# Optimization experiments

Hardware: AMD Instinct MI355X
Metric: run time of the kernel (lower is better)

## Reference

```python
import jax, jax.numpy as jnp
import numpy as np
import math

D = 768
H = 8
DK = D // H
FF = 1024
EPS = 1e-5


def _layer_norm(x, g, b):
    m = jnp.mean(x, axis=-1, keepdims=True)
    v = jnp.mean((x - m) ** 2, axis=-1, keepdims=True)
    return (x - m) * jax.lax.rsqrt(v + EPS) * g + b


def _mha(x, attention_mask, Wq, bq, Wv, bv, g, b):
    # x: (B,S,D); attention_mask: (B,S,1) bool (True = masked/padding query row)
    B, S, _ = x.shape
    q = (x @ Wq + bq).reshape(B, S, H, DK).transpose(0, 2, 1, 3)  # (B,H,S,dk)
    # NOTE: original code uses the V projection for BOTH k and v (k = self.V(x))
    kv = (x @ Wv + bv).reshape(B, S, H, DK).transpose(0, 2, 1, 3)
    k = kv
    v = kv
    w = jnp.einsum('bhqd,bhkd->bhqk', q, k) / math.sqrt(DK)  # (B,H,S,S)
    pad = attention_mask[:, None, :, :]                      # (B,1,S,1) -> bcast (B,1,S,S)
    causal = jnp.triu(jnp.ones((S, S), dtype=bool), k=1)     # look-ahead mask
    mask = pad | causal
    w = jnp.where(mask, jnp.float32(-1e9), w)
    # NOTE: original uses nn.Softmax(dim=2) -> softmax over the QUERY axis
    score = jax.nn.softmax(w, axis=2)
    o = jnp.einsum('bhqk,bhkd->bhqd', score, v)              # (B,H,S,dk)
    o = o.transpose(0, 2, 1, 3).reshape(B, S, D)
    return _layer_norm(o + x, g, b)


def _ffn(x, W1, b1, W2, b2, g, b):
    h = jax.nn.relu(x @ W1 + b1)
    return _layer_norm(h @ W2 + b2 + x, g, b)


def setup_inputs() -> dict:
    key = jax.random.key(0)
    ks = jax.random.split(key, 16)
    B, S = 8, 1024
    sc = 0.02
    inp = {
        'x': jax.random.normal(ks[0], (B, S, D), dtype=jnp.float32),
        'attention_mask': jax.random.randint(ks[1], (B, S, 1), 0, 2).astype(bool),
    }
    for i, pre in enumerate(['a1', 'a2']):
        inp[pre + '_Wq'] = jax.random.normal(ks[2 + 4 * i], (D, D), dtype=jnp.float32) * sc
        inp[pre + '_bq'] = jnp.zeros((D,), dtype=jnp.float32)
        inp[pre + '_Wv'] = jax.random.normal(ks[3 + 4 * i], (D, D), dtype=jnp.float32) * sc
        inp[pre + '_bv'] = jnp.zeros((D,), dtype=jnp.float32)
        inp[pre + '_g'] = jnp.ones((D,), dtype=jnp.float32)
        inp[pre + '_b'] = jnp.zeros((D,), dtype=jnp.float32)
    inp['f_W1'] = jax.random.normal(ks[10], (D, FF), dtype=jnp.float32) * sc
    inp['f_b1'] = jnp.zeros((FF,), dtype=jnp.float32)
    inp['f_W2'] = jax.random.normal(ks[11], (FF, D), dtype=jnp.float32) * sc
    inp['f_b2'] = jnp.zeros((D,), dtype=jnp.float32)
    inp['f_g'] = jnp.ones((D,), dtype=jnp.float32)
    inp['f_b'] = jnp.zeros((D,), dtype=jnp.float32)
    return inp


def reference(x, attention_mask,
              a1_Wq, a1_bq, a1_Wv, a1_bv, a1_g, a1_b,
              a2_Wq, a2_bq, a2_Wv, a2_bv, a2_g, a2_b,
              f_W1, f_b1, f_W2, f_b2, f_g, f_b):
    x = _mha(x, attention_mask, a1_Wq, a1_bq, a1_Wv, a1_bv, a1_g, a1_b)
    x = _mha(x, attention_mask, a2_Wq, a2_bq, a2_Wv, a2_bv, a2_g, a2_b)
    x = _ffn(x, f_W1, f_b1, f_W2, f_b2, f_g, f_b)
    return x
```

## Files before the change

### kernel.cpp

```cpp
#include <hip/hip_runtime.h>
#include <cstddef>

#define BB 8
#define SS 1024
#define DD 768
#define HH 8
#define DKK 96
#define FFF 1024
#define MM (BB*SS)
#define QVW 1536
#define SM_SCALE 0.10206207261596577f
#define NT2 8

typedef unsigned short ushort_t;
typedef short short8 __attribute__((ext_vector_type(8)));
typedef float f32x4 __attribute__((ext_vector_type(4)));
typedef float f32x16 __attribute__((ext_vector_type(16)));
typedef ushort_t us4 __attribute__((ext_vector_type(4)));
typedef unsigned uint2v __attribute__((ext_vector_type(2)));

__device__ __forceinline__ ushort_t f2b(float f) {
    union { float f; unsigned u; } x; x.f = f;
    unsigned r = x.u + 0x7fffu + ((x.u >> 16) & 1u);
    return (ushort_t)(r >> 16);
}
__device__ __forceinline__ float b2f(ushort_t u) {
    union { unsigned u; float f; } x; x.u = ((unsigned)u) << 16;
    return x.f;
}
__device__ __forceinline__ void gload16(const ushort_t* g, void* lds_base) {
    __builtin_amdgcn_global_load_lds(
        (const __attribute__((address_space(1))) unsigned int*)g,
        (__attribute__((address_space(3))) unsigned int*)lds_base, 16, 0, 0);
}
__device__ __forceinline__ void plswap(unsigned& a, unsigned& b) {
#if __has_builtin(__builtin_amdgcn_permlane32_swap)
    uint2v r = __builtin_amdgcn_permlane32_swap(a, b, false, false);
    a = r[0]; b = r[1];
#else
    asm("v_permlane32_swap_b32 %0, %1" : "+v"(a), "+v"(b));
#endif
}

__device__ __forceinline__ void castWT_body(
    const float* __restrict__ W, ushort_t* __restrict__ Wt,
    int K, int N, int bx, int by)
{
    __shared__ float T[32][33];
    const int tx = threadIdx.x & 31, ty = threadIdx.x >> 5;
    const int n0 = bx * 32, k0 = by * 32;
    #pragma unroll
    for (int r = 0; r < 4; ++r)
        T[ty + 8*r][tx] = W[(size_t)(k0 + ty + 8*r) * N + n0 + tx];
    __syncthreads();
    #pragma unroll
    for (int r = 0; r < 4; ++r)
        Wt[(size_t)(n0 + ty + 8*r) * K + k0 + tx] = f2b(T[tx][ty + 8*r]);
}

__global__ __launch_bounds__(256) void prep_all(
    const float* __restrict__ Wqa, const float* __restrict__ Wva,
    const float* __restrict__ Wqb, const float* __restrict__ Wvb,
    ushort_t* __restrict__ Tqa, ushort_t* __restrict__ Tva,
    ushort_t* __restrict__ Tqb, ushort_t* __restrict__ Tvb,
    const float* __restrict__ W1, ushort_t* __restrict__ T1,
    const float* __restrict__ W2, ushort_t* __restrict__ T2,
    const float* __restrict__ x, ushort_t* __restrict__ xb)
{
    const int id = blockIdx.x;
    if (id < 2304) {
        const int z = id / 576, r = id % 576;
        const float* W = (z == 0) ? Wqa : (z == 1) ? Wva : (z == 2) ? Wqb : Wvb;
        ushort_t* Wt   = (z == 0) ? Tqa : (z == 1) ? Tva : (z == 2) ? Tqb : Tvb;
        castWT_body(W, Wt, DD, DD, r % 24, r / 24);
    } else if (id < 3072) {
        const int r = id - 2304;
        castWT_body(W1, T1, DD, FFF, r % 32, r / 32);
    } else if (id < 3840) {
        const int r = id - 3072;
        castWT_body(W2, T2, FFF, DD, r % 24, r / 24);
    } else {
        const int i = (id - 3840) * 256 + threadIdx.x;
        const float4 v = ((const float4*)x)[i];
        us4 o; o.x = f2b(v.x); o.y = f2b(v.y); o.z = f2b(v.z); o.w = f2b(v.w);
        ((us4*)xb)[i] = o;
    }
}

template<int RELU>
__global__ __launch_bounds__(256) void gemm_bt(
    const ushort_t* __restrict__ A, const ushort_t* __restrict__ Bt,
    const float* __restrict__ bias, const float* __restrict__ bias2, int bN,
    ushort_t* __restrict__ C, int K, int N)
{
    __shared__ ushort_t S[128*136];
    ushort_t* As = S;
    ushort_t* Bs = S + 128*64;
    const int tid  = threadIdx.x;
    const int lane = tid & 63, wave = tid >> 6;
    const int wm = wave >> 1, wn = wave & 1;
    const int n = lane & 15, quad = lane >> 4;
    const int sx = n & 7;
    const int nbx = N >> 7;
    const int cpx = gridDim.x >> 3;
    const int sw  = (blockIdx.x & 7) * cpx + (blockIdx.x >> 3);
    const int bm = (sw / nbx) * 128, bn = (sw % nbx) * 128;

    f32x4 acc[4][4];
    #pragma unroll
    for (int i = 0; i < 4; ++i)
        #pragma unroll
        for (int j = 0; j < 4; ++j) acc[i][j] = (f32x4){0.f, 0.f, 0.f, 0.f};

    for (int k0 = 0; k0 < K; k0 += 64) {
        #pragma unroll
        for (int it = 0; it < 4; ++it) {
            const int u   = (it*4 + wave)*64 + lane;
            const int row = u >> 3;
            const int c   = (u & 7) ^ (row & 7);
            gload16(A  + (size_t)(bm + row) * K + k0 + c*8, (char*)As + (it*4 + wave)*1024);
            gload16(Bt + (size_t)(bn + row) * K + k0 + c*8, (char*)Bs + (it*4 + wave)*1024);
        }
        __syncthreads();
        #pragma unroll
        for (int ks = 0; ks < 2; ++ks) {
            short8 af[4], bf[4];
            #pragma unroll
            for (int i = 0; i < 4; ++i)
                af[i] = *(short8*)&As[((wm*64 + i*16 + n)*8 + ((ks*4 + quad) ^ sx))*8];
            #pragma unroll
            for (int j = 0; j < 4; ++j)
                bf[j] = *(short8*)&Bs[((wn*64 + j*16 + n)*8 + ((ks*4 + quad) ^ sx))*8];
            __builtin_amdgcn_s_setprio(1);
            #pragma unroll
            for (int i = 0; i < 4; ++i)
                #pragma unroll
                for (int j = 0; j < 4; ++j)
                    acc[i][j] = __builtin_amdgcn_mfma_f32_16x16x32_bf16(af[i], bf[j], acc[i][j], 0, 0, 0);
            __builtin_amdgcn_s_setprio(0);
        }
        __syncthreads();
    }
    #pragma unroll
    for (int j = 0; j < 4; ++j) {
        const int col = wn*64 + j*16 + n;
        const int gcol = bn + col;
        const float bsv = (gcol < bN) ? bias[gcol] : bias2[gcol - bN];
        #pragma unroll
        for (int i = 0; i < 4; ++i) {
            const int lrow = wm*64 + i*16 + quad*4;
            #pragma unroll
            for (int r = 0; r < 4; ++r) {
                float v = acc[i][j][r] + bsv;
                if (RELU) v = fmaxf(v, 0.f);
                S[(lrow + r)*136 + col] = f2b(v);
            }
        }
    }
    __syncthreads();
    #pragma unroll
    for (int it = 0; it < 8; ++it) {
        const int u = it*256 + tid;
        const int grow = u >> 4, gc = u & 15;
        *(short8*)(C + (size_t)(bm + grow)*N + bn + gc*8) = *(short8*)&S[grow*136 + gc*8];
    }
}

__global__ __launch_bounds__(512) void attn_sums(
    const ushort_t* __restrict__ QV, const int* __restrict__ amask,
    float* __restrict__ lpart)
{
    __shared__ ushort_t Qs[128*128];
    __shared__ ushort_t Ks[2][64*128];
    __shared__ float colsum[2][8][64];
    const int tid = threadIdx.x, lane = tid & 63, wave = tid >> 6;
    const int n = lane & 15, quad = lane >> 4, sx = n & 7;
    const int hwid = blockIdx.x;
    const int v = (hwid & 7) * 32 + (hwid >> 3);
    const int px = v & 3, h = (v >> 2) & 7, b = v >> 5;
    const ushort_t* Qh = QV + (size_t)b*SS*QVW + h*DKK;
    const ushort_t* Kh = QV + (size_t)b*SS*QVW + DD + h*DKK;
    float* lpq = lpart + (size_t)(b*HH + h)*NT2*SS;

    #pragma unroll
    for (int half = 0; half < 2; ++half) {
        const int qt2 = half ? (7 - px) : px;
        const int q0 = qt2 * 128;
        const int ktmax = 2*qt2 + 1;
        #pragma unroll
        for (int it = 0; it < 4; ++it) {
            const int u = (it*8 + wave)*64 + lane;
            const int row = u >> 4, c = (u & 15) ^ (row & 7);
            if (c < 12)
                gload16(Qh + (size_t)(q0 + row)*QVW + c*8, (char*)Qs + (it*8 + wave)*1024);
        }
        const int4 mv = *(const int4*)&amask[b*SS + q0 + wave*16 + quad*4];
        const int mr[4] = {mv.x, mv.y, mv.z, mv.w};
        #pragma unroll
        for (int it = 0; it < 2; ++it) {
            const int u = (it*8 + wave)*64 + lane;
            const int row = u >> 4, c = (u & 15) ^ (row & 7);
            if (c < 12)
                gload16(Kh + (size_t)row*QVW + c*8, (char*)Ks[0] + (it*8 + wave)*1024);
        }
        __syncthreads();
        short8 aq[3];
        #pragma unroll
        for (int ks = 0; ks < 3; ++ks)
            aq[ks] = *(short8*)&Qs[((wave*16 + n)*16 + ((ks*4 + quad) ^ sx))*8];

        int cur = 0;
        for (int kt = 0; kt <= ktmax; ++kt) {
            const int k0 = kt * 64;
            if (kt < ktmax) {
                #pragma unroll
                for (int it = 0; it < 2; ++it) {
                    const int u = (it*8 + wave)*64 + lane;
                    const int row = u >> 4, c = (u & 15) ^ (row & 7);
                    if (c < 12)
                        gload16(Kh + (size_t)(k0 + 64 + row)*QVW + c*8,
                                (char*)Ks[cur^1] + (it*8 + wave)*1024);
                }
            }
            if (kt > 0 && tid < 64) {
                const float s = colsum[cur^1][0][tid] + colsum[cur^1][1][tid]
                              + colsum[cur^1][2][tid] + colsum[cur^1][3][tid]
                              + colsum[cur^1][4][tid] + colsum[cur^1][5][tid]
                              + colsum[cur^1][6][tid] + colsum[cur^1][7][tid];
                lpq[(size_t)qt2*SS + (k0 - 64) + tid] = s;
            }
            #pragma unroll
            for (int ns = 0; ns < 4; ++ns) {
                f32x4 sa = (f32x4){0.f, 0.f, 0.f, 0.f};
                __builtin_amdgcn_s_setprio(1);
                #pragma unroll
                for (int ks = 0; ks < 3; ++ks) {
                    const short8 bk = *(short8*)&Ks[cur][((ns*16 + n)*16 + ((ks*4 + quad) ^ sx))*8];
                    sa = __builtin_amdgcn_mfma_f32_16x16x32_bf16(aq[ks], bk, sa, 0, 0, 0);
                }
                __builtin_amdgcn_s_setprio(0);
                const int kl = ns*16 + n;
                const int keyg = k0 + kl;
                float s = 0.f;
                #pragma unroll
                for (int r = 0; r < 4; ++r) {
                    const int qg = q0 + wave*16 + quad*4 + r;
                    const bool dead = (mr[r] != 0) || (keyg > qg);
                    s += dead ? 0.f : __expf(sa[r] * SM_SCALE);
                }
                s += __shfl_xor(s, 16);
                s += __shfl_xor(s, 32);
                if (quad == 0) colsum[cur][wave][kl] = s;
            }
            __syncthreads();
            cur ^= 1;
        }
        if (tid < 64) {
            const int pb = ktmax & 1;
            const float s = colsum[pb][0][tid] + colsum[pb][1][tid]
                          + colsum[pb][2][tid] + colsum[pb][3][tid]
                          + colsum[pb][4][tid] + colsum[pb][5][tid]
                          + colsum[pb][6][tid] + colsum[pb][7][tid];
            lpq[(size_t)qt2*SS + ktmax*64 + tid] = s;
        }
    }
}

__global__ __launch_bounds__(256) void transpose_scale(
    const ushort_t* __restrict__ QV, const float* __restrict__ lpart,
    ushort_t* __restrict__ Vt)
{
    __shared__ ushort_t T[64][104];
    __shared__ float rlv[64];
    const int tid = threadIdx.x;
    const int k0 = blockIdx.x * 64, h = blockIdx.y, b = blockIdx.z;
    const ushort_t* src = QV + (size_t)b*SS*QVW + DD + h*DKK;
    for (int s = tid; s < 768; s += 256) {
        const int r = s / 12, c = s % 12;
        *(short8*)&T[r][c*8] = *(const short8*)(src + (size_t)(k0 + r)*QVW + c*8);
    }
    if (tid < 64) {
        const float* lp = lpart + (size_t)(b*HH + h)*NT2*SS;
        float l = 0.f;
        for (int qt2 = k0 >> 7; qt2 < NT2; ++qt2) l += lp[(size_t)qt2*SS + k0 + tid];
        rlv[tid] = (l > 0.f) ? (1.f / l) : 0.f;
    }
    __syncthreads();
    ushort_t* dst = Vt + ((size_t)b*HH + h)*DKK*SS;
    for (int s = tid; s < 768; s += 256) {
        const int dk = s >> 3, c = s & 7;
        short8 v;
        #pragma unroll
        for (int i = 0; i < 8; ++i)
            v[i] = (short)f2b(b2f(T[c*8 + i][dk]) * rlv[c*8 + i]);
        *(short8*)(dst + (size_t)dk*SS + k0 + c*8) = v;
    }
}

__global__ __launch_bounds__(256, 2) void attn_pv_re(
    const ushort_t* __restrict__ QV, const int* __restrict__ amask,
    const ushort_t* __restrict__ Vt, ushort_t* __restrict__ O)
{
    __shared__ ushort_t Ks[2][64*128];
    __shared__ ushort_t Vs[2][96*64];
    const int tid = threadIdx.x, lane = tid & 63, wave = tid >> 6;
    const int ln31 = lane & 31, hi = lane >> 5;
    const int hwid = blockIdx.x;
    const int v = (hwid & 7) * 32 + (hwid >> 3);
    const int px = v & 3, h = (v >> 2) & 7, b = v >> 5;
    const ushort_t* Qh = QV + (size_t)b*SS*QVW + h*DKK;
    const ushort_t* Kh = QV + (size_t)b*SS*QVW + DD + h*DKK;
    const ushort_t* Vth = Vt + ((size_t)b*HH + h)*DKK*SS;

    #pragma unroll
    for (int half = 0; half < 2; ++half) {
        const int qt2 = half ? (7 - px) : px;
        const int q0 = qt2 * 128;
        const int ktmax = 2*qt2 + 1;
        const int qrow = q0 + wave*32 + ln31;
        short8 bq[6];
        #pragma unroll
        for (int t = 0; t < 6; ++t)
            bq[t] = *(const short8*)(Qh + (size_t)qrow*QVW + t*16 + hi*8);
        const bool padq = amask[b*SS + qrow] != 0;

        #pragma unroll
        for (int it = 0; it < 4; ++it) {
            const int u = (it*4 + wave)*64 + lane;
            const int row = u >> 4, c = (u & 15) ^ (row & 7);
            if (c < 12)
                gload16(Kh + (size_t)row*QVW + c*8, (char*)Ks[0] + (it*4 + wave)*1024);
        }
        #pragma unroll
        for (int it = 0; it < 3; ++it) {
            const int u = (it*4 + wave)*64 + lane;
            const int row = u >> 3, c = (u & 7) ^ (row & 7);
            gload16(Vth + (size_t)row*SS + c*8, (char*)Vs[0] + (it*4 + wave)*1024);
        }
        __syncthreads();

        f32x16 acc[3];
        #pragma unroll
        for (int db = 0; db < 3; ++db)
            #pragma unroll
            for (int i = 0; i < 16; ++i) acc[db][i] = 0.f;

        int cur = 0;
        for (int kt = 0; kt <= ktmax; ++kt) {
            const int k0 = kt * 64;
            if (kt < ktmax) {
                #pragma unroll
                for (int it = 0; it < 4; ++it) {
                    const int u = (it*4 + wave)*64 + lane;
                    const int row = u >> 4, c = (u & 15) ^ (row & 7);
                    if (c < 12)
                        gload16(Kh + (size_t)(k0 + 64 + row)*QVW + c*8,
                                (char*)Ks[cur^1] + (it*4 + wave)*1024);
                }
                #pragma unroll
                for (int it = 0; it < 3; ++it) {
                    const int u = (it*4 + wave)*64 + lane;
                    const int row = u >> 3, c = (u & 7) ^ (row & 7);
                    gload16(Vth + (size_t)row*SS + k0 + 64 + c*8,
                            (char*)Vs[cur^1] + (it*4 + wave)*1024);
                }
            }
            #pragma unroll
            for (int kb = 0; kb < 2; ++kb) {
                f32x16 sk;
                #pragma unroll
                for (int i = 0; i < 16; ++i) sk[i] = 0.f;
                const int krow = kb*32 + ln31;
                __builtin_amdgcn_s_setprio(1);
                #pragma unroll
                for (int t = 0; t < 6; ++t) {
                    const short8 ak = *(short8*)&Ks[cur][krow*128 + (((t*2 + hi) ^ (krow & 7))*8)];
                    sk = __builtin_amdgcn_mfma_f32_32x32x16_bf16(ak, bq[t], sk, 0, 0, 0);
                }
                __builtin_amdgcn_s_setprio(0);
                const int kbase = k0 + kb*32 + 4*hi;
                float p[16];
                #pragma unroll
                for (int r = 0; r < 16; ++r) {
                    const int kg = kbase + (r & 3) + 8*(r >> 2);
                    const bool dead = padq || (kg > qrow);
                    p[r] = dead ? 0.f : __expf(sk[r] * SM_SCALE);
                }
                unsigned w[8];
                #pragma unroll
                for (int i = 0; i < 8; ++i)
                    asm("v_cvt_pk_bf16_f32 %0, %1, %2" : "=v"(w[i]) : "v"(p[2*i]), "v"(p[2*i+1]));
                plswap(w[0], w[2]);
                plswap(w[1], w[3]);
                plswap(w[4], w[6]);
                plswap(w[5], w[7]);
                __builtin_amdgcn_s_setprio(1);
                #pragma unroll
                for (int s = 0; s < 2; ++s) {
                    short8 ae;
                    unsigned* aeu = (unsigned*)&ae;
                    aeu[0] = w[s*4 + 0]; aeu[1] = w[s*4 + 1];
                    aeu[2] = w[s*4 + 2]; aeu[3] = w[s*4 + 3];
                    #pragma unroll
                    for (int db = 0; db < 3; ++db) {
                        const int drow = db*32 + ln31;
                        const short8 bv = *(short8*)&Vs[cur][drow*64 + (((kb*4 + s*2 + hi) ^ (drow & 7))*8)];
                        acc[db] = __builtin_amdgcn_mfma_f32_32x32x16_bf16(ae, bv, acc[db], 0, 0, 0);
                    }
                }
                __builtin_amdgcn_s_setprio(0);
            }
            __syncthreads();
            cur ^= 1;
        }
        #pragma unroll
        for (int db = 0; db < 3; ++db) {
            #pragma unroll
            for (int r = 0; r < 16; ++r) {
                const int q = q0 + wave*32 + (r & 3) + 8*(r >> 2) + 4*hi;
                O[((size_t)b*SS + q)*DD + h*DKK + db*32 + ln31] = f2b(acc[db][r]);
            }
        }
    }
}

__device__ __forceinline__ float block_sum256(float s, float* tmp4)
{
    #pragma unroll
    for (int off = 32; off > 0; off >>= 1) s += __shfl_down(s, off);
    __syncthreads();
    if ((threadIdx.x & 63) == 0) tmp4[threadIdx.x >> 6] = s;
    __syncthreads();
    return tmp4[0] + tmp4[1] + tmp4[2] + tmp4[3];
}

template<int XBF, int RBF, int OUTF32>
__global__ __launch_bounds__(256) void resid_ln(
    const void* __restrict__ X, const void* __restrict__ R,
    const float* __restrict__ g, const float* __restrict__ beta,
    ushort_t* __restrict__ OutB, float* __restrict__ OutF)
{
    __shared__ float tmp4[4];
    const int row = blockIdx.x;
    const int tid = threadIdx.x;
    float v[3], s = 0.f;
    #pragma unroll
    for (int i = 0; i < 3; ++i) {
        const size_t idx = (size_t)row * DD + tid + 256*i;
        const float xv = XBF ? b2f(((const ushort_t*)X)[idx]) : ((const float*)X)[idx];
        const float rv = RBF ? b2f(((const ushort_t*)R)[idx]) : ((const float*)R)[idx];
        v[i] = xv + rv;
        s += v[i];
    }
    const float mu = block_sum256(s, tmp4) * (1.f / DD);
    float qv = 0.f;
    #pragma unroll
    for (int i = 0; i < 3; ++i) { const float d = v[i] - mu; qv += d * d; }
    const float inv = rsqrtf(block_sum256(qv, tmp4) * (1.f / DD) + 1e-5f);
    #pragma unroll
    for (int i = 0; i < 3; ++i) {
        const int c = tid + 256*i;
        const float o = (v[i] - mu) * inv * g[c] + beta[c];
        if (OUTF32) OutF[(size_t)row * DD + c] = o;
        else        OutB[(size_t)row * DD + c] = f2b(o);
    }
}

extern "C" void kernel_launch(void* const* d_in, const int* in_sizes, int n_in,
                              void* d_out, int out_size, void* d_ws, size_t ws_size,
                              hipStream_t stream)
{
    (void)in_sizes; (void)n_in; (void)out_size; (void)ws_size;
    const float* x0    = (const float*)d_in[0];
    const int*   amask = (const int*)d_in[1];
    const float* a1_Wq = (const float*)d_in[2];
    const float* a1_bq = (const float*)d_in[3];
    const float* a1_Wv = (const float*)d_in[4];
    const float* a1_bv = (const float*)d_in[5];
    const float* a1_g  = (const float*)d_in[6];
    const float* a1_b  = (const float*)d_in[7];
    const float* a2_Wq = (const float*)d_in[8];
    const float* a2_bq = (const float*)d_in[9];
    const float* a2_Wv = (const float*)d_in[10];
    const float* a2_bv = (const float*)d_in[11];
    const float* a2_g  = (const float*)d_in[12];
    const float* a2_b  = (const float*)d_in[13];
    const float* f_W1  = (const float*)d_in[14];
    const float* f_b1  = (const float*)d_in[15];
    const float* f_W2  = (const float*)d_in[16];
    const float* f_b2  = (const float*)d_in[17];
    const float* f_g   = (const float*)d_in[18];
    const float* f_b   = (const float*)d_in[19];

    char* ws = (char*)d_ws;
    size_t off = 0;
    auto alloc = [&](size_t bytes) { void* p = ws + off; off += (bytes + 255) & ~(size_t)255; return p; };
    ushort_t* WqvT1 = (ushort_t*)alloc((size_t)QVW*DD*2);
    ushort_t* WqvT2 = (ushort_t*)alloc((size_t)QVW*DD*2);
    ushort_t* W1T   = (ushort_t*)alloc((size_t)DD*FFF*2);
    ushort_t* W2T   = (ushort_t*)alloc((size_t)DD*FFF*2);
    ushort_t* xb0   = (ushort_t*)alloc((size_t)MM*DD*2);
    ushort_t* xb1   = (ushort_t*)alloc((size_t)MM*DD*2);
    ushort_t* xb2   = (ushort_t*)alloc((size_t)MM*DD*2);
    ushort_t* Ob    = (ushort_t*)alloc((size_t)MM*DD*2);
    ushort_t* QVb   = (ushort_t*)alloc((size_t)MM*QVW*2);
    ushort_t* hb    = QVb;
    ushort_t* Vtb   = (ushort_t*)alloc((size_t)MM*DD*2);
    float* lpart = (float*)alloc((size_t)BB*HH*NT2*SS*4);
    float* out = (float*)d_out;

    const dim3 blk(256);
    const dim3 blk512(512);
    const dim3 gat(256);
    const dim3 gtr(SS/64, HH, BB);

    prep_all<<<dim3(9984), blk, 0, stream>>>(
        a1_Wq, a1_Wv, a2_Wq, a2_Wv,
        WqvT1, WqvT1 + (size_t)DD*DD, WqvT2, WqvT2 + (size_t)DD*DD,
        f_W1, W1T, f_W2, W2T, x0, xb0);

    gemm_bt<0><<<dim3((QVW/128)*(MM/128)), blk, 0, stream>>>(xb0, WqvT1, a1_bq, a1_bv, DD, QVb, DD, QVW);
    attn_sums<<<gat, blk512, 0, stream>>>(QVb, amask, lpart);
    transpose_scale<<<gtr, blk, 0, stream>>>(QVb, lpart, Vtb);
    attn_pv_re<<<gat, blk, 0, stream>>>(QVb, amask, Vtb, Ob);
    resid_ln<1,0,0><<<dim3(MM), blk, 0, stream>>>(Ob, x0, a1_g, a1_b, xb1, nullptr);

    gemm_bt<0><<<dim3((QVW/128)*(MM/128)), blk, 0, stream>>>(xb1, WqvT2, a2_bq, a2_bv, DD, QVb, DD, QVW);
    attn_sums<<<gat, blk512, 0, stream>>>(QVb, amask, lpart);
    transpose_scale<<<gtr, blk, 0, stream>>>(QVb, lpart, Vtb);
    attn_pv_re<<<gat, blk, 0, stream>>>(QVb, amask, Vtb, Ob);
    resid_ln<1,1,0><<<dim3(MM), blk, 0, stream>>>(Ob, xb1, a2_g, a2_b, xb2, nullptr);

    gemm_bt<1><<<dim3((FFF/128)*(MM/128)), blk, 0, stream>>>(xb2, W1T, f_b1, f_b1, FFF, hb, DD, FFF);
    gemm_bt<0><<<dim3((DD/128)*(MM/128)), blk, 0, stream>>>(hb, W2T, f_b2, f_b2, DD, Ob, FFF, DD);
    resid_ln<1,1,1><<<dim3(MM), blk, 0, stream>>>(Ob, xb2, f_g, f_b, nullptr, out);
}
```

Before: 382.7 us.

## Write transposed V from QV GEMM epilogue and apply column normalizer in PV kernel

```diff
diff --git a/kernel.cpp b/kernel.cpp
--- a/kernel.cpp
+++ b/kernel.cpp
@@ -87,11 +87,11 @@
     }
 }
 
-template<int RELU>
+template<int RELU, int WVT>
 __global__ __launch_bounds__(256) void gemm_bt(
     const ushort_t* __restrict__ A, const ushort_t* __restrict__ Bt,
     const float* __restrict__ bias, const float* __restrict__ bias2, int bN,
-    ushort_t* __restrict__ C, int K, int N)
+    ushort_t* __restrict__ C, int K, int N, ushort_t* __restrict__ Vt)
 {
     __shared__ ushort_t S[128*136];
     ushort_t* As = S;
@@ -156,6 +156,20 @@
                 S[(lrow + r)*136 + col] = f2b(v);
             }
         }
+        if (WVT && bn >= DD) {
+            const int gkv = gcol - DD;
+            const int hh = gkv / DKK, dk = gkv % DKK;
+            ushort_t* vt = Vt + ((size_t)((bm >> 10)*HH + hh)*DKK + dk)*SS + (bm & 1023);
+            #pragma unroll
+            for (int i = 0; i < 4; ++i) {
+                us4 o;
+                o.x = f2b(acc[i][j][0] + bsv);
+                o.y = f2b(acc[i][j][1] + bsv);
+                o.z = f2b(acc[i][j][2] + bsv);
+                o.w = f2b(acc[i][j][3] + bsv);
+                *(us4*)(vt + wm*64 + i*16 + quad*4) = o;
+            }
+        }
     }
     __syncthreads();
     #pragma unroll
@@ -266,43 +280,33 @@
     }
 }
 
-__global__ __launch_bounds__(256) void transpose_scale(
-    const ushort_t* __restrict__ QV, const float* __restrict__ lpart,
-    ushort_t* __restrict__ Vt)
-{
-    __shared__ ushort_t T[64][104];
-    __shared__ float rlv[64];
-    const int tid = threadIdx.x;
-    const int k0 = blockIdx.x * 64, h = blockIdx.y, b = blockIdx.z;
-    const ushort_t* src = QV + (size_t)b*SS*QVW + DD + h*DKK;
-    for (int s = tid; s < 768; s += 256) {
-        const int r = s / 12, c = s % 12;
-        *(short8*)&T[r][c*8] = *(const short8*)(src + (size_t)(k0 + r)*QVW + c*8);
-    }
-    if (tid < 64) {
-        const float* lp = lpart + (size_t)(b*HH + h)*NT2*SS;
-        float l = 0.f;
-        for (int qt2 = k0 >> 7; qt2 < NT2; ++qt2) l += lp[(size_t)qt2*SS + k0 + tid];
-        rlv[tid] = (l > 0.f) ? (1.f / l) : 0.f;
-    }
-    __syncthreads();
-    ushort_t* dst = Vt + ((size_t)b*HH + h)*DKK*SS;
-    for (int s = tid; s < 768; s += 256) {
-        const int dk = s >> 3, c = s & 7;
-        short8 v;
-        #pragma unroll
-        for (int i = 0; i < 8; ++i)
-            v[i] = (short)f2b(b2f(T[c*8 + i][dk]) * rlv[c*8 + i]);
-        *(short8*)(dst + (size_t)dk*SS + k0 + c*8) = v;
-    }
-}
-
-__global__ __launch_bounds__(256, 2) void attn_pv_re(
+__global__ __launch_bounds__(256) void mk_rl(
+    const float* __restrict__ lpart, float* __restrict__ rl)
+{
+    const int bh = blockIdx.x;
+    const float* lp = lpart + (size_t)bh*NT2*SS;
+    const int k = threadIdx.x * 4;
+    const int qtmin = k >> 7;
+    float4 l = {0.f, 0.f, 0.f, 0.f};
+    for (int q = qtmin; q < NT2; ++q) {
+        const float4 v = *(const float4*)(lp + (size_t)q*SS + k);
+        l.x += v.x; l.y += v.y; l.z += v.z; l.w += v.w;
+    }
+    float4 r;
+    r.x = (l.x > 0.f) ? (1.f / l.x) : 0.f;
+    r.y = (l.y > 0.f) ? (1.f / l.y) : 0.f;
+    r.z = (l.z > 0.f) ? (1.f / l.z) : 0.f;
+    r.w = (l.w > 0.f) ? (1.f / l.w) : 0.f;
+    *(float4*)(rl + (size_t)bh*SS + k) = r;
+}
+
+__global__ __launch_bounds__(256, 3) void attn_pv_re(
     const ushort_t* __restrict__ QV, const int* __restrict__ amask,
-    const ushort_t* __restrict__ Vt, ushort_t* __restrict__ O)
+    const ushort_t* __restrict__ Vt, const float* __restrict__ rl,
+    ushort_t* __restrict__ O)
 {
     __shared__ ushort_t Ks[2][64*128];
-    __shared__ ushort_t Vs[2][96*64];
+    __shared__ ushort_t Vs[96*64];
     const int tid = threadIdx.x, lane = tid & 63, wave = tid >> 6;
     const int ln31 = lane & 31, hi = lane >> 5;
     const int hwid = blockIdx.x;
@@ -311,6 +315,7 @@
     const ushort_t* Qh = QV + (size_t)b*SS*QVW + h*DKK;
     const ushort_t* Kh = QV + (size_t)b*SS*QVW + DD + h*DKK;
     const ushort_t* Vth = Vt + ((size_t)b*HH + h)*DKK*SS;
+    const float* rlh = rl + ((size_t)b*HH + h)*SS;
 
     #pragma unroll
     for (int half = 0; half < 2; ++half) {
@@ -335,7 +340,7 @@
         for (int it = 0; it < 3; ++it) {
             const int u = (it*4 + wave)*64 + lane;
             const int row = u >> 3, c = (u & 7) ^ (row & 7);
-            gload16(Vth + (size_t)row*SS + c*8, (char*)Vs[0] + (it*4 + wave)*1024);
+            gload16(Vth + (size_t)row*SS + c*8, (char*)Vs + (it*4 + wave)*1024);
         }
         __syncthreads();
 
@@ -357,60 +362,70 @@
                         gload16(Kh + (size_t)(k0 + 64 + row)*QVW + c*8,
                                 (char*)Ks[cur^1] + (it*4 + wave)*1024);
                 }
+            }
+            unsigned wv[2][8];
+            #pragma unroll
+            for (int kb = 0; kb < 2; ++kb) {
+                f32x16 sk;
+                #pragma unroll
+                for (int i = 0; i < 16; ++i) sk[i] = 0.f;
+                const int krow = kb*32 + ln31;
+                __builtin_amdgcn_s_setprio(1);
+                #pragma unroll
+                for (int t = 0; t < 6; ++t) {
+                    const short8 ak = *(short8*)&Ks[cur][krow*128 + (((t*2 + hi) ^ (krow & 7))*8)];
+                    sk = __builtin_amdgcn_mfma_f32_32x32x16_bf16(ak, bq[t], sk, 0, 0, 0);
+                }
+                __builtin_amdgcn_s_setprio(0);
+                const int kbase = k0 + kb*32 + 4*hi;
+                float4 r4[4];
+                #pragma unroll
+                for (int m = 0; m < 4; ++m)
+                    r4[m] = *(const float4*)(rlh + kbase + 8*m);
+                float p[16];
+                #pragma unroll
+                for (int r = 0; r < 16; ++r) {
+                    const int kg = kbase + (r & 3) + 8*(r >> 2);
+                    const bool dead = padq || (kg > qrow);
+                    const float rs = (&r4[r >> 2].x)[r & 3];
+                    p[r] = dead ? 0.f : __expf(sk[r] * SM_SCALE) * rs;
+                }
+                #pragma unroll
+                for (int i = 0; i < 8; ++i)
+                    asm("v_cvt_pk_bf16_f32 %0, %1, %2" : "=v"(wv[kb][i]) : "v"(p[2*i]), "v"(p[2*i+1]));
+                plswap(wv[kb][0], wv[kb][2]);
+                plswap(wv[kb][1], wv[kb][3]);
+                plswap(wv[kb][4], wv[kb][6]);
+                plswap(wv[kb][5], wv[kb][7]);
+            }
+            __syncthreads();
+            __builtin_amdgcn_s_setprio(1);
+            #pragma unroll
+            for (int kb = 0; kb < 2; ++kb) {
+                #pragma unroll
+                for (int s = 0; s < 2; ++s) {
+                    short8 ae;
+                    unsigned* aeu = (unsigned*)&ae;
+                    aeu[0] = wv[kb][s*4 + 0]; aeu[1] = wv[kb][s*4 + 1];
+                    aeu[2] = wv[kb][s*4 + 2]; aeu[3] = wv[kb][s*4 + 3];
+                    #pragma unroll
+                    for (int db = 0; db < 3; ++db) {
+                        const int drow = db*32 + ln31;
+                        const short8 bv = *(short8*)&Vs[drow*64 + (((kb*4 + s*2 + hi) ^ (drow & 7))*8)];
+                        acc[db] = __builtin_amdgcn_mfma_f32_32x32x16_bf16(ae, bv, acc[db], 0, 0, 0);
+                    }
+                }
+            }
+            __builtin_amdgcn_s_setprio(0);
+            __syncthreads();
+            if (kt < ktmax) {
                 #pragma unroll
                 for (int it = 0; it < 3; ++it) {
                     const int u = (it*4 + wave)*64 + lane;
                     const int row = u >> 3, c = (u & 7) ^ (row & 7);
-                    gload16(Vth + (size_t)row*SS + k0 + 64 + c*8,
-                            (char*)Vs[cur^1] + (it*4 + wave)*1024);
-                }
-            }
-            #pragma unroll
-            for (int kb = 0; kb < 2; ++kb) {
-                f32x16 sk;
-                #pragma unroll
-                for (int i = 0; i < 16; ++i) sk[i] = 0.f;
-                const int krow = kb*32 + ln31;
-                __builtin_amdgcn_s_setprio(1);
-                #pragma unroll
-                for (int t = 0; t < 6; ++t) {
-                    const short8 ak = *(short8*)&Ks[cur][krow*128 + (((t*2 + hi) ^ (krow & 7))*8)];
-                    sk = __builtin_amdgcn_mfma_f32_32x32x16_bf16(ak, bq[t], sk, 0, 0, 0);
-                }
-                __builtin_amdgcn_s_setprio(0);
-                const int kbase = k0 + kb*32 + 4*hi;
-                float p[16];
-                #pragma unroll
-                for (int r = 0; r < 16; ++r) {
-                    const int kg = kbase + (r & 3) + 8*(r >> 2);
-                    const bool dead = padq || (kg > qrow);
-                    p[r] = dead ? 0.f : __expf(sk[r] * SM_SCALE);
-                }
-                unsigned w[8];
-                #pragma unroll
-                for (int i = 0; i < 8; ++i)
-                    asm("v_cvt_pk_bf16_f32 %0, %1, %2" : "=v"(w[i]) : "v"(p[2*i]), "v"(p[2*i+1]));
-                plswap(w[0], w[2]);
-                plswap(w[1], w[3]);
-                plswap(w[4], w[6]);
-                plswap(w[5], w[7]);
-                __builtin_amdgcn_s_setprio(1);
-                #pragma unroll
-                for (int s = 0; s < 2; ++s) {
-                    short8 ae;
-                    unsigned* aeu = (unsigned*)&ae;
-                    aeu[0] = w[s*4 + 0]; aeu[1] = w[s*4 + 1];
-                    aeu[2] = w[s*4 + 2]; aeu[3] = w[s*4 + 3];
-                    #pragma unroll
-                    for (int db = 0; db < 3; ++db) {
-                        const int drow = db*32 + ln31;
-                        const short8 bv = *(short8*)&Vs[cur][drow*64 + (((kb*4 + s*2 + hi) ^ (drow & 7))*8)];
-                        acc[db] = __builtin_amdgcn_mfma_f32_32x32x16_bf16(ae, bv, acc[db], 0, 0, 0);
-                    }
-                }
-                __builtin_amdgcn_s_setprio(0);
-            }
-            __syncthreads();
+                    gload16(Vth + (size_t)row*SS + k0 + 64 + c*8, (char*)Vs + (it*4 + wave)*1024);
+                }
+            }
             cur ^= 1;
         }
         #pragma unroll
@@ -507,31 +522,31 @@
     ushort_t* hb    = QVb;
     ushort_t* Vtb   = (ushort_t*)alloc((size_t)MM*DD*2);
     float* lpart = (float*)alloc((size_t)BB*HH*NT2*SS*4);
+    float* rlb   = (float*)alloc((size_t)BB*HH*SS*4);
     float* out = (float*)d_out;
 
     const dim3 blk(256);
     const dim3 blk512(512);
     const dim3 gat(256);
-    const dim3 gtr(SS/64, HH, BB);
 
     prep_all<<<dim3(9984), blk, 0, stream>>>(
         a1_Wq, a1_Wv, a2_Wq, a2_Wv,
         WqvT1, WqvT1 + (size_t)DD*DD, WqvT2, WqvT2 + (size_t)DD*DD,
         f_W1, W1T, f_W2, W2T, x0, xb0);
 
-    gemm_bt<0><<<dim3((QVW/128)*(MM/128)), blk, 0, stream>>>(xb0, WqvT1, a1_bq, a1_bv, DD, QVb, DD, QVW);
+    gemm_bt<0,1><<<dim3((QVW/128)*(MM/128)), blk, 0, stream>>>(xb0, WqvT1, a1_bq, a1_bv, DD, QVb, DD, QVW, Vtb);
     attn_sums<<<gat, blk512, 0, stream>>>(QVb, amask, lpart);
-    transpose_scale<<<gtr, blk, 0, stream>>>(QVb, lpart, Vtb);
-    attn_pv_re<<<gat, blk, 0, stream>>>(QVb, amask, Vtb, Ob);
+    mk_rl<<<dim3(BB*HH), blk, 0, stream>>>(lpart, rlb);
+    attn_pv_re<<<gat, blk, 0, stream>>>(QVb, amask, Vtb, rlb, Ob);
     resid_ln<1,0,0><<<dim3(MM), blk, 0, stream>>>(Ob, x0, a1_g, a1_b, xb1, nullptr);
 
-    gemm_bt<0><<<dim3((QVW/128)*(MM/128)), blk, 0, stream>>>(xb1, WqvT2, a2_bq, a2_bv, DD, QVb, DD, QVW);
+    gemm_bt<0,1><<<dim3((QVW/128)*(MM/128)), blk, 0, stream>>>(xb1, WqvT2, a2_bq, a2_bv, DD, QVb, DD, QVW, Vtb);
     attn_sums<<<gat, blk512, 0, stream>>>(QVb, amask, lpart);
-    transpose_scale<<<gtr, blk, 0, stream>>>(QVb, lpart, Vtb);
-    attn_pv_re<<<gat, blk, 0, stream>>>(QVb, amask, Vtb, Ob);
+    mk_rl<<<dim3(BB*HH), blk, 0, stream>>>(lpart, rlb);
+    attn_pv_re<<<gat, blk, 0, stream>>>(QVb, amask, Vtb, rlb, Ob);
     resid_ln<1,1,0><<<dim3(MM), blk, 0, stream>>>(Ob, xb1, a2_g, a2_b, xb2, nullptr);
 
-    gemm_bt<1><<<dim3((FFF/128)*(MM/128)), blk, 0, stream>>>(xb2, W1T, f_b1, f_b1, FFF, hb, DD, FFF);
-    gemm_bt<0><<<dim3((DD/128)*(MM/128)), blk, 0, stream>>>(hb, W2T, f_b2, f_b2, DD, Ob, FFF, DD);
+    gemm_bt<1,0><<<dim3((FFF/128)*(MM/128)), blk, 0, stream>>>(xb2, W1T, f_b1, f_b1, FFF, hb, DD, FFF, nullptr);
+    gemm_bt<0,0><<<dim3((DD/128)*(MM/128)), blk, 0, stream>>>(hb, W2T, f_b2, f_b2, DD, Ob, FFF, DD, nullptr);
     resid_ln<1,1,1><<<dim3(MM), blk, 0, stream>>>(Ob, xb2, f_g, f_b, nullptr, out);
 }
```

Result: slower. 446.2 us (+16.6%).
